# Kernel tuning notes

Hardware: AMD Instinct MI355X
Metric: run time of the kernel (lower is better)

Reference implementation:

```python
import jax, jax.numpy as jnp
import numpy as np

H = 1024
S = 2048
B = 16

def setup_inputs() -> dict:
    key = jax.random.key(0)
    k1, k2, k3, k4, k5, k6 = jax.random.split(key, 6)
    hidden = jax.random.normal(k1, (1, B, H), dtype=jnp.float32)
    encoder_outputs = jax.random.normal(k2, (S, B, H), dtype=jnp.float32)
    seq_mask = jax.random.randint(k3, (B, S), 0, 2, dtype=jnp.int32)
    # nn.Linear(2H, H): weight [H, 2H], bias [H]
    lim1 = 1.0 / np.sqrt(2 * H)
    attn_w = jax.random.uniform(k4, (H, 2 * H), minval=-lim1, maxval=lim1, dtype=jnp.float32)
    attn_b = jax.random.uniform(k5, (H,), minval=-lim1, maxval=lim1, dtype=jnp.float32)
    # nn.Linear(H, 1, bias=False): weight [1, H]
    lim2 = 1.0 / np.sqrt(H)
    score_w = jax.random.uniform(k6, (1, H), minval=-lim2, maxval=lim2, dtype=jnp.float32)
    return {"hidden": hidden, "encoder_outputs": encoder_outputs, "seq_mask": seq_mask,
            "attn_w": attn_w, "attn_b": attn_b, "score_w": score_w}

def reference(hidden, encoder_outputs, seq_mask, attn_w, attn_b, score_w):
    # Faithful to: cat([hidden.repeat(S,1,1), encoder_outputs], -1) @ attn_w.T + attn_b
    # Split the concat-linear into two GEMMs (identical math, avoids the big concat).
    h = hidden.shape[-1]
    Wh = attn_w[:, :h]   # acts on repeated hidden
    We = attn_w[:, h:]   # acts on encoder outputs
    # hidden: [1,B,H] broadcasts over S; encoder_outputs: [S,B,H]
    pre = jnp.einsum('obh,kh->obk', hidden, Wh) + jnp.einsum('sbh,kh->sbk', encoder_outputs, We) + attn_b
    proj = jnp.tanh(pre)                               # [S,B,H]
    energies = jnp.einsum('sbh,oh->sbo', proj, score_w)[..., 0]  # [S,B]
    energies = energies.T                              # [B,S] (transpose(0,1) in original)
    energies = jnp.where(seq_mask.astype(bool), jnp.float32(-1e12), energies)
    attn = jax.nn.softmax(energies, axis=1)            # [B,S]
    return attn[:, None, :]                            # [B,1,S]
```

## Files before the change

kernel.cpp:

```cpp
#include <hip/hip_runtime.h>
#include <hip/hip_bf16.h>

#define HDIM 1024
#define SEQ 2048
#define BATCH 16
#define M_TOT (SEQ*BATCH)
#define NBLK 4
#define BM 256
#define BN 256
#define BKT 64
#define NT (HDIM/BKT)

#define NB_ENC ((M_TOT*HDIM)/(8*256))
#define NB_WE  ((HDIM*HDIM)/(8*256))
#define NB_QK  (HDIM)

typedef __attribute__((ext_vector_type(8))) short short8;
typedef __attribute__((ext_vector_type(4))) float f32x4;

typedef const void __attribute__((address_space(1))) gvoid_t;
typedef void __attribute__((address_space(3))) svoid_t;
#define GLD16(gp, lp) __builtin_amdgcn_global_load_lds((gvoid_t*)(gp), (svoid_t*)(lp), 16, 0, 0)
#define VMC(N) asm volatile("s_waitcnt vmcnt(" #N ")" ::: "memory")

static __device__ __forceinline__ unsigned short f2bf(float f) {
    unsigned int x = __float_as_uint(f);
    unsigned int r = (x + 0x7FFFu + ((x >> 16) & 1u)) >> 16;
    return (unsigned short)r;
}

__global__ __launch_bounds__(256) void prep_all(const float* __restrict__ hidden,
                                                const float* __restrict__ enc,
                                                const float* __restrict__ attn_w,
                                                const float* __restrict__ attn_b,
                                                float* __restrict__ q,
                                                __hip_bfloat16* __restrict__ web,
                                                __hip_bfloat16* __restrict__ encb) {
    int bid = blockIdx.x;
    if (bid < NB_ENC) {
        size_t i0 = ((size_t)bid * 256 + threadIdx.x) * 8;
        const float4* s = reinterpret_cast<const float4*>(enc + i0);
        float4 a = s[0], b = s[1];
        union { unsigned short u[8]; short8 v; } cv;
        cv.u[0] = f2bf(a.x); cv.u[1] = f2bf(a.y); cv.u[2] = f2bf(a.z); cv.u[3] = f2bf(a.w);
        cv.u[4] = f2bf(b.x); cv.u[5] = f2bf(b.y); cv.u[6] = f2bf(b.z); cv.u[7] = f2bf(b.w);
        *reinterpret_cast<short8*>((unsigned short*)encb + i0) = cv.v;
        return;
    }
    if (bid < NB_ENC + NB_WE) {
        size_t i0 = ((size_t)(bid - NB_ENC) * 256 + threadIdx.x) * 8;
        int n = (int)(i0 >> 10);
        int h = (int)(i0 & 1023);
        const float4* src = reinterpret_cast<const float4*>(attn_w + (size_t)n * (2 * HDIM) + HDIM + h);
        float4 a = src[0], b = src[1];
        union { unsigned short u[8]; short8 v; } cv;
        cv.u[0] = f2bf(a.x); cv.u[1] = f2bf(a.y); cv.u[2] = f2bf(a.z); cv.u[3] = f2bf(a.w);
        cv.u[4] = f2bf(b.x); cv.u[5] = f2bf(b.y); cv.u[6] = f2bf(b.z); cv.u[7] = f2bf(b.w);
        *reinterpret_cast<short8*>((unsigned short*)web + i0) = cv.v;
        return;
    }
    int k = bid - (NB_ENC + NB_WE);
    int tid = threadIdx.x;
    const float* w = attn_w + (size_t)k * (2 * HDIM);
    float p[BATCH];
#pragma unroll
    for (int b = 0; b < BATCH; b++) p[b] = 0.f;
    for (int h = tid; h < HDIM; h += 256) {
        float wv = w[h];
#pragma unroll
        for (int b = 0; b < BATCH; b++) p[b] += hidden[b * HDIM + h] * wv;
    }
#pragma unroll
    for (int b = 0; b < BATCH; b++) {
        for (int off = 32; off; off >>= 1) p[b] += __shfl_down(p[b], off);
    }
    __shared__ float red[4][BATCH];
    int lane = tid & 63, wid = tid >> 6;
    if (lane == 0) {
#pragma unroll
        for (int b = 0; b < BATCH; b++) red[wid][b] = p[b];
    }
    __syncthreads();
    if (tid < BATCH) {
        float s = red[0][tid] + red[1][tid] + red[2][tid] + red[3][tid] + attn_b[k];
        q[(size_t)tid * HDIM + k] = s;
    }
}

__global__ __launch_bounds__(512, 2) void gemm8(const __hip_bfloat16* __restrict__ encb,
                                                const __hip_bfloat16* __restrict__ web,
                                                const float* __restrict__ qv,
                                                const float* __restrict__ score_w,
                                                float* __restrict__ part) {
    __shared__ __align__(16) char pool[131072];

    int tid = threadIdx.x;
    int lane = tid & 63;
    int wid = tid >> 6;
    int wr = wid >> 2;
    int wc = wid & 3;

    int bid = blockIdx.x;
    int lin = (bid & 7) * 64 + (bid >> 3);
    int bm = lin >> 2;
    int bn = lin & 3;
    int m0 = bm * BM, n0 = bn * BN;

    int srow = tid >> 3;
    int scolb = (((tid & 7) ^ ((tid >> 3) & 7)) << 4);
    const char* eb = (const char*)encb;
    const char* wb = (const char*)web;

    auto STG = [&](const char* g, int ldsoff) {
        GLD16(g + (size_t)srow * 2048 + scolb, pool + ldsoff + wid * 1024);
        GLD16(g + (size_t)(srow + 64) * 2048 + scolb, pool + ldsoff + 8192 + wid * 1024);
    };
    auto APTR = [&](int kt, int h) { return eb + ((size_t)(m0 + h * 128) * HDIM + kt * BKT) * 2; };
    auto BPTR = [&](int kt, int h) { return wb + ((size_t)(n0 + h * 128) * HDIM + kt * BKT) * 2; };
#define ALDS(par, h) ((par) * 32768 + (h) * 16384)
#define BLDS(par, h) (65536 + (par) * 32768 + (h) * 16384)

    int lq = lane & 15, lh = lane >> 4;
    int flip = (lane & 7) << 4;
    int pks0 = lq * 128 + ((lh * 16) ^ flip);
    int pks1 = lq * 128 + (((64 + lh * 16)) ^ flip);
    int aFB = wr * 16384;
    int bFB = 65536 + (wc >> 1) * 16384 + (wc & 1) * 8192;

    f32x4 acc[8][4];
#pragma unroll
    for (int i = 0; i < 8; i++)
#pragma unroll
        for (int j = 0; j < 4; j++) acc[i][j] = (f32x4)0.f;
    short8 br[4][2];

#define RD8(off) (*reinterpret_cast<const short8*>(pool + (off)))

#define PHASE(Q, PAR, STAGE_STMT, PRE_CLOSE)                                              \
    {                                                                                     \
        if ((Q) == 0) {                                                                   \
            _Pragma("unroll") for (int nj = 0; nj < 4; ++nj) {                            \
                br[nj][0] = RD8(bFB + (PAR) * 32768 + nj * 2048 + pks0);                  \
                br[nj][1] = RD8(bFB + (PAR) * 32768 + nj * 2048 + pks1);                  \
            }                                                                             \
        }                                                                                 \
        short8 a0k0 = RD8(aFB + (PAR) * 32768 + (2 * (Q)) * 2048 + pks0);                 \
        short8 a0k1 = RD8(aFB + (PAR) * 32768 + (2 * (Q)) * 2048 + pks1);                 \
        short8 a1k0 = RD8(aFB + (PAR) * 32768 + (2 * (Q) + 1) * 2048 + pks0);             \
        short8 a1k1 = RD8(aFB + (PAR) * 32768 + (2 * (Q) + 1) * 2048 + pks1);             \
        STAGE_STMT;                                                                       \
        __builtin_amdgcn_s_barrier();                                                     \
        __builtin_amdgcn_s_setprio(1);                                                    \
        _Pragma("unroll") for (int nj = 0; nj < 4; ++nj) {                                \
            acc[2 * (Q)][nj] = __builtin_amdgcn_mfma_f32_16x16x32_bf16(a0k0, br[nj][0], acc[2 * (Q)][nj], 0, 0, 0); \
            acc[2 * (Q)][nj] = __builtin_amdgcn_mfma_f32_16x16x32_bf16(a0k1, br[nj][1], acc[2 * (Q)][nj], 0, 0, 0); \
            acc[2 * (Q) + 1][nj] = __builtin_amdgcn_mfma_f32_16x16x32_bf16(a1k0, br[nj][0], acc[2 * (Q) + 1][nj], 0, 0, 0); \
            acc[2 * (Q) + 1][nj] = __builtin_amdgcn_mfma_f32_16x16x32_bf16(a1k1, br[nj][1], acc[2 * (Q) + 1][nj], 0, 0, 0); \
        }                                                                                 \
        __builtin_amdgcn_s_setprio(0);                                                    \
        PRE_CLOSE;                                                                        \
        __builtin_amdgcn_s_barrier();                                                     \
        __builtin_amdgcn_sched_barrier(0);                                                \
    }

    STG(BPTR(0, 0), BLDS(0, 0));
    STG(BPTR(0, 1), BLDS(0, 1));
    STG(APTR(0, 0), ALDS(0, 0));
    STG(APTR(0, 1), ALDS(0, 1));
    STG(BPTR(1, 0), BLDS(1, 0));
    STG(BPTR(1, 1), BLDS(1, 1));
    VMC(4);
    __builtin_amdgcn_s_barrier();
    __builtin_amdgcn_sched_barrier(0);

#pragma unroll 1
    for (int J = 0; J < 7; ++J) {
        int k1 = 2 * J + 1;
        PHASE(0, 0, STG(APTR(k1, 0), ALDS(1, 0)), );
        PHASE(1, 0, STG(APTR(k1, 1), ALDS(1, 1)), );
        PHASE(2, 0, STG(BPTR(k1 + 1, 0), BLDS(0, 0)), );
        PHASE(3, 0, STG(BPTR(k1 + 1, 1), BLDS(0, 1)), VMC(4));
        PHASE(0, 1, STG(APTR(k1 + 1, 0), ALDS(0, 0)), );
        PHASE(1, 1, STG(APTR(k1 + 1, 1), ALDS(0, 1)), );
        PHASE(2, 1, STG(BPTR(k1 + 2, 0), BLDS(1, 0)), );
        PHASE(3, 1, STG(BPTR(k1 + 2, 1), BLDS(1, 1)), VMC(4));
    }
    PHASE(0, 0, STG(APTR(15, 0), ALDS(1, 0)), );
    PHASE(1, 0, STG(APTR(15, 1), ALDS(1, 1)), );
    PHASE(2, 0, , );
    PHASE(3, 0, , VMC(0));
    PHASE(0, 1, , );
    PHASE(1, 1, , );
    PHASE(2, 1, , );
    PHASE(3, 1, , );

    float* q_lds = reinterpret_cast<float*>(pool);
    float* sc_lds = reinterpret_cast<float*>(pool + 16384);
    float* eng = reinterpret_cast<float*>(pool + 17408);
    {
        int qb = tid >> 5;
        int kl = (tid & 31) * 8;
        const float4* src = reinterpret_cast<const float4*>(qv + (size_t)qb * HDIM + n0 + kl);
        float4 v0 = src[0], v1 = src[1];
        *reinterpret_cast<float4*>(&q_lds[qb * 256 + kl]) = v0;
        *reinterpret_cast<float4*>(&q_lds[qb * 256 + kl + 4]) = v1;
        if (tid < BN) sc_lds[tid] = score_w[n0 + tid];
    }
    __syncthreads();

#pragma unroll
    for (int mi = 0; mi < 8; ++mi) {
#pragma unroll
        for (int r = 0; r < 4; ++r) {
            int b = lh * 4 + r;
            float s = 0.f;
#pragma unroll
            for (int nj = 0; nj < 4; ++nj) {
                int kl = wc * 64 + nj * 16 + lq;
                float v = acc[mi][nj][r] + q_lds[b * 256 + kl];
                float t = 1.f - 2.f / (__expf(2.f * v) + 1.f);
                s += sc_lds[kl] * t;
            }
            for (int off = 1; off < 16; off <<= 1) s += __shfl_xor(s, off);
            if (lq == 0) eng[wc * 256 + wr * 128 + mi * 16 + b] = s;
        }
    }
    __syncthreads();
    if (tid < BM) {
        float s = eng[tid] + eng[256 + tid] + eng[512 + tid] + eng[768 + tid];
        part[(size_t)bn * M_TOT + m0 + tid] = s;
    }
#undef PHASE
#undef RD8
#undef ALDS
#undef BLDS
}

__global__ __launch_bounds__(256) void softmax_kernel(const float* __restrict__ part,
                                                      const int* __restrict__ mask,
                                                      float* __restrict__ out) {
    int b = blockIdx.x;
    int tid = threadIdx.x;
    __shared__ float e_lds[SEQ];
    __shared__ float red[4], red2[4];
    int lane = tid & 63, wid = tid >> 6;
    float lmax = -3.4e38f;
    for (int it = 0; it < SEQ / 256; ++it) {
        int s = it * 256 + tid;
        size_t m = (size_t)s * BATCH + b;
        float e = 0.f;
#pragma unroll
        for (int c = 0; c < NBLK; c++) e += part[(size_t)c * M_TOT + m];
        if (mask[(size_t)b * SEQ + s]) e = -1e12f;
        e_lds[s] = e;
        lmax = fmaxf(lmax, e);
    }
    for (int off = 32; off; off >>= 1) lmax = fmaxf(lmax, __shfl_xor(lmax, off));
    if (lane == 0) red[wid] = lmax;
    __syncthreads();
    float gmax = fmaxf(fmaxf(red[0], red[1]), fmaxf(red[2], red[3]));
    float lsum = 0.f;
    for (int it = 0; it < SEQ / 256; ++it) {
        int s = it * 256 + tid;
        float p = __expf(e_lds[s] - gmax);
        e_lds[s] = p;
        lsum += p;
    }
    for (int off = 32; off; off >>= 1) lsum += __shfl_xor(lsum, off);
    if (lane == 0) red2[wid] = lsum;
    __syncthreads();
    float inv = 1.f / (red2[0] + red2[1] + red2[2] + red2[3]);
    for (int it = 0; it < SEQ / 256; ++it) {
        int s = it * 256 + tid;
        out[(size_t)b * SEQ + s] = e_lds[s] * inv;
    }
}

extern "C" void kernel_launch(void* const* d_in, const int* in_sizes, int n_in,
                              void* d_out, int out_size, void* d_ws, size_t ws_size,
                              hipStream_t stream) {
    const float* hidden   = (const float*)d_in[0];
    const float* enc      = (const float*)d_in[1];
    const int*   seq_mask = (const int*)d_in[2];
    const float* attn_w   = (const float*)d_in[3];
    const float* attn_b   = (const float*)d_in[4];
    const float* score_w  = (const float*)d_in[5];
    float* out = (float*)d_out;

    char* ws = (char*)d_ws;
    float* q = (float*)ws;
    __hip_bfloat16* web = (__hip_bfloat16*)(ws + 65536);
    float* part = (float*)(ws + 65536 + 2 * 1024 * 1024);
    __hip_bfloat16* encb = (__hip_bfloat16*)(ws + 65536 + 3 * 1024 * 1024);

    prep_all<<<dim3(NB_ENC + NB_WE + NB_QK), dim3(256), 0, stream>>>(hidden, enc, attn_w, attn_b, q, web, encb);
    gemm8<<<dim3(NBLK * (M_TOT / BM)), dim3(512), 0, stream>>>(encb, web, q, score_w, part);
    softmax_kernel<<<dim3(BATCH), dim3(256), 0, stream>>>(part, seq_mask, out);
}
```

Before: 120.7 us.

## Fuse fp32-to-bf16 encoder conversion into GEMM via fp32 LDS staging

Removes the separate pass that converts the 128 MB fp32 encoder tensor to bf16. The GEMM now streams fp32 encoder tiles directly into LDS and converts them to bf16 in registers before the MFMAs. To fit this it halves the K tile to 32, uses a triple-buffered pipeline and enlarges LDS to 144 KB. This drops one full read and a write-back of the encoder, at the price of twice the A-tile load bytes per GEMM and extra conversion ALU work. Because four N-blocks each re-read the fp32 A rows, global traffic grows, and the larger LDS footprint may limit occupancy.

```diff
diff --git a/kernel.cpp b/kernel.cpp
--- a/kernel.cpp
+++ b/kernel.cpp
@@ -8,10 +8,9 @@
 #define NBLK 4
 #define BM 256
 #define BN 256
-#define BKT 64
-#define NT (HDIM/BKT)
-
-#define NB_ENC ((M_TOT*HDIM)/(8*256))
+#define BKT 32
+#define NTT (HDIM/BKT)
+
 #define NB_WE  ((HDIM*HDIM)/(8*256))
 #define NB_QK  (HDIM)
 
@@ -30,25 +29,13 @@
 }
 
 __global__ __launch_bounds__(256) void prep_all(const float* __restrict__ hidden,
-                                                const float* __restrict__ enc,
                                                 const float* __restrict__ attn_w,
                                                 const float* __restrict__ attn_b,
                                                 float* __restrict__ q,
-                                                __hip_bfloat16* __restrict__ web,
-                                                __hip_bfloat16* __restrict__ encb) {
+                                                __hip_bfloat16* __restrict__ web) {
     int bid = blockIdx.x;
-    if (bid < NB_ENC) {
+    if (bid < NB_WE) {
         size_t i0 = ((size_t)bid * 256 + threadIdx.x) * 8;
-        const float4* s = reinterpret_cast<const float4*>(enc + i0);
-        float4 a = s[0], b = s[1];
-        union { unsigned short u[8]; short8 v; } cv;
-        cv.u[0] = f2bf(a.x); cv.u[1] = f2bf(a.y); cv.u[2] = f2bf(a.z); cv.u[3] = f2bf(a.w);
-        cv.u[4] = f2bf(b.x); cv.u[5] = f2bf(b.y); cv.u[6] = f2bf(b.z); cv.u[7] = f2bf(b.w);
-        *reinterpret_cast<short8*>((unsigned short*)encb + i0) = cv.v;
-        return;
-    }
-    if (bid < NB_ENC + NB_WE) {
-        size_t i0 = ((size_t)(bid - NB_ENC) * 256 + threadIdx.x) * 8;
         int n = (int)(i0 >> 10);
         int h = (int)(i0 & 1023);
         const float4* src = reinterpret_cast<const float4*>(attn_w + (size_t)n * (2 * HDIM) + HDIM + h);
@@ -59,7 +46,7 @@
         *reinterpret_cast<short8*>((unsigned short*)web + i0) = cv.v;
         return;
     }
-    int k = bid - (NB_ENC + NB_WE);
+    int k = bid - NB_WE;
     int tid = threadIdx.x;
     const float* w = attn_w + (size_t)k * (2 * HDIM);
     float p[BATCH];
@@ -87,12 +74,12 @@
     }
 }
 
-__global__ __launch_bounds__(512, 2) void gemm8(const __hip_bfloat16* __restrict__ encb,
+__global__ __launch_bounds__(512, 2) void gemm8(const float* __restrict__ enc,
                                                 const __hip_bfloat16* __restrict__ web,
                                                 const float* __restrict__ qv,
                                                 const float* __restrict__ score_w,
                                                 float* __restrict__ part) {
-    __shared__ __align__(16) char pool[131072];
+    __shared__ __align__(16) char pool[147456];
 
     int tid = threadIdx.x;
     int lane = tid & 63;
@@ -106,93 +93,108 @@
     int bn = lin & 3;
     int m0 = bm * BM, n0 = bn * BN;
 
-    int srow = tid >> 3;
-    int scolb = (((tid & 7) ^ ((tid >> 3) & 7)) << 4);
-    const char* eb = (const char*)encb;
-    const char* wb = (const char*)web;
-
-    auto STG = [&](const char* g, int ldsoff) {
-        GLD16(g + (size_t)srow * 2048 + scolb, pool + ldsoff + wid * 1024);
-        GLD16(g + (size_t)(srow + 64) * 2048 + scolb, pool + ldsoff + 8192 + wid * 1024);
+    const char* encB = (const char*)enc;
+    const char* webB = (const char*)web;
+
+    int arow_l = wid * 16 + (lane >> 3);
+    int agsw = ((lane & 7) ^ (lane >> 3)) << 4;
+    auto ASTG = [&](int t, int h, int ab) {
+        const char* g0 = encB + (((size_t)(m0 + h * 128 + arow_l) * HDIM + t * BKT) << 2) + agsw;
+        GLD16(g0, pool + ab * 32768 + h * 16384 + wid * 2048);
+        GLD16(g0 + (8u * HDIM << 2), pool + ab * 32768 + h * 16384 + wid * 2048 + 1024);
     };
-    auto APTR = [&](int kt, int h) { return eb + ((size_t)(m0 + h * 128) * HDIM + kt * BKT) * 2; };
-    auto BPTR = [&](int kt, int h) { return wb + ((size_t)(n0 + h * 128) * HDIM + kt * BKT) * 2; };
-#define ALDS(par, h) ((par) * 32768 + (h) * 16384)
-#define BLDS(par, h) (65536 + (par) * 32768 + (h) * 16384)
-
-    int lq = lane & 15, lh = lane >> 4;
-    int flip = (lane & 7) << 4;
-    int pks0 = lq * 128 + ((lh * 16) ^ flip);
-    int pks1 = lq * 128 + (((64 + lh * 16)) ^ flip);
-    int aFB = wr * 16384;
-    int bFB = 65536 + (wc >> 1) * 16384 + (wc & 1) * 8192;
+
+    int brow_l = wid * 16 + (lane >> 2);
+    int bgsw = ((lane & 3) ^ ((lane >> 2) & 3)) << 4;
+    auto BSTG = [&](int t, int h, int bb) {
+        const char* g0 = webB + (((size_t)(n0 + h * 128 + brow_l) * HDIM + t * BKT) << 1) + bgsw;
+        GLD16(g0, pool + 98304 + bb * 16384 + h * 8192 + wid * 1024);
+    };
+
+    int lq = lane & 15, kb = lane >> 4;
+    int aRB = wr * 16384 + lq * 128;
+    int aS0 = ((2 * kb) ^ (lq & 7)) << 4;
+    int aS1 = ((2 * kb + 1) ^ (lq & 7)) << 4;
+    int bRB = 98304 + (wc >> 1) * 8192 + ((wc & 1) * 64 + lq) * 64;
+    int bS = (kb ^ (lq & 3)) << 4;
 
     f32x4 acc[8][4];
 #pragma unroll
     for (int i = 0; i < 8; i++)
 #pragma unroll
         for (int j = 0; j < 4; j++) acc[i][j] = (f32x4)0.f;
-    short8 br[4][2];
+    short8 br[4];
 
 #define RD8(off) (*reinterpret_cast<const short8*>(pool + (off)))
-
-#define PHASE(Q, PAR, STAGE_STMT, PRE_CLOSE)                                              \
+#define RDF(off) (*reinterpret_cast<const f32x4*>(pool + (off)))
+
+    auto CVT = [&](f32x4 lo, f32x4 hi) {
+        union { __hip_bfloat162 b[4]; short8 s; } u;
+        u.b[0] = __float22bfloat162_rn(make_float2(lo[0], lo[1]));
+        u.b[1] = __float22bfloat162_rn(make_float2(lo[2], lo[3]));
+        u.b[2] = __float22bfloat162_rn(make_float2(hi[0], hi[1]));
+        u.b[3] = __float22bfloat162_rn(make_float2(hi[2], hi[3]));
+        return u.s;
+    };
+
+#define PH1(T, AB, SB, DOSTG)                                                             \
     {                                                                                     \
-        if ((Q) == 0) {                                                                   \
-            _Pragma("unroll") for (int nj = 0; nj < 4; ++nj) {                            \
-                br[nj][0] = RD8(bFB + (PAR) * 32768 + nj * 2048 + pks0);                  \
-                br[nj][1] = RD8(bFB + (PAR) * 32768 + nj * 2048 + pks1);                  \
-            }                                                                             \
-        }                                                                                 \
-        short8 a0k0 = RD8(aFB + (PAR) * 32768 + (2 * (Q)) * 2048 + pks0);                 \
-        short8 a0k1 = RD8(aFB + (PAR) * 32768 + (2 * (Q)) * 2048 + pks1);                 \
-        short8 a1k0 = RD8(aFB + (PAR) * 32768 + (2 * (Q) + 1) * 2048 + pks0);             \
-        short8 a1k1 = RD8(aFB + (PAR) * 32768 + (2 * (Q) + 1) * 2048 + pks1);             \
-        STAGE_STMT;                                                                       \
+        _Pragma("unroll") for (int nj = 0; nj < 4; ++nj)                                  \
+            br[nj] = RD8(bRB + (AB) * 16384 + nj * 1024 + bS);                            \
+        short8 af0 = CVT(RDF((AB) * 32768 + aRB + 0 * 2048 + aS0), RDF((AB) * 32768 + aRB + 0 * 2048 + aS1)); \
+        short8 af1 = CVT(RDF((AB) * 32768 + aRB + 1 * 2048 + aS0), RDF((AB) * 32768 + aRB + 1 * 2048 + aS1)); \
+        short8 af2 = CVT(RDF((AB) * 32768 + aRB + 2 * 2048 + aS0), RDF((AB) * 32768 + aRB + 2 * 2048 + aS1)); \
+        short8 af3 = CVT(RDF((AB) * 32768 + aRB + 3 * 2048 + aS0), RDF((AB) * 32768 + aRB + 3 * 2048 + aS1)); \
+        if (DOSTG) { ASTG((T) + 2, 0, SB); BSTG((T) + 2, 0, SB); }                        \
         __builtin_amdgcn_s_barrier();                                                     \
         __builtin_amdgcn_s_setprio(1);                                                    \
         _Pragma("unroll") for (int nj = 0; nj < 4; ++nj) {                                \
-            acc[2 * (Q)][nj] = __builtin_amdgcn_mfma_f32_16x16x32_bf16(a0k0, br[nj][0], acc[2 * (Q)][nj], 0, 0, 0); \
-            acc[2 * (Q)][nj] = __builtin_amdgcn_mfma_f32_16x16x32_bf16(a0k1, br[nj][1], acc[2 * (Q)][nj], 0, 0, 0); \
-            acc[2 * (Q) + 1][nj] = __builtin_amdgcn_mfma_f32_16x16x32_bf16(a1k0, br[nj][0], acc[2 * (Q) + 1][nj], 0, 0, 0); \
-            acc[2 * (Q) + 1][nj] = __builtin_amdgcn_mfma_f32_16x16x32_bf16(a1k1, br[nj][1], acc[2 * (Q) + 1][nj], 0, 0, 0); \
+            acc[0][nj] = __builtin_amdgcn_mfma_f32_16x16x32_bf16(af0, br[nj], acc[0][nj], 0, 0, 0); \
+            acc[1][nj] = __builtin_amdgcn_mfma_f32_16x16x32_bf16(af1, br[nj], acc[1][nj], 0, 0, 0); \
+            acc[2][nj] = __builtin_amdgcn_mfma_f32_16x16x32_bf16(af2, br[nj], acc[2][nj], 0, 0, 0); \
+            acc[3][nj] = __builtin_amdgcn_mfma_f32_16x16x32_bf16(af3, br[nj], acc[3][nj], 0, 0, 0); \
         }                                                                                 \
         __builtin_amdgcn_s_setprio(0);                                                    \
-        PRE_CLOSE;                                                                        \
         __builtin_amdgcn_s_barrier();                                                     \
         __builtin_amdgcn_sched_barrier(0);                                                \
     }
 
-    STG(BPTR(0, 0), BLDS(0, 0));
-    STG(BPTR(0, 1), BLDS(0, 1));
-    STG(APTR(0, 0), ALDS(0, 0));
-    STG(APTR(0, 1), ALDS(0, 1));
-    STG(BPTR(1, 0), BLDS(1, 0));
-    STG(BPTR(1, 1), BLDS(1, 1));
-    VMC(4);
+#define PH2(T, AB, SB, DOSTG, CLOSE)                                                      \
+    {                                                                                     \
+        short8 af4 = CVT(RDF((AB) * 32768 + aRB + 4 * 2048 + aS0), RDF((AB) * 32768 + aRB + 4 * 2048 + aS1)); \
+        short8 af5 = CVT(RDF((AB) * 32768 + aRB + 5 * 2048 + aS0), RDF((AB) * 32768 + aRB + 5 * 2048 + aS1)); \
+        short8 af6 = CVT(RDF((AB) * 32768 + aRB + 6 * 2048 + aS0), RDF((AB) * 32768 + aRB + 6 * 2048 + aS1)); \
+        short8 af7 = CVT(RDF((AB) * 32768 + aRB + 7 * 2048 + aS0), RDF((AB) * 32768 + aRB + 7 * 2048 + aS1)); \
+        if (DOSTG) { ASTG((T) + 2, 1, SB); BSTG((T) + 2, 1, SB); }                        \
+        __builtin_amdgcn_s_barrier();                                                     \
+        __builtin_amdgcn_s_setprio(1);                                                    \
+        _Pragma("unroll") for (int nj = 0; nj < 4; ++nj) {                                \
+            acc[4][nj] = __builtin_amdgcn_mfma_f32_16x16x32_bf16(af4, br[nj], acc[4][nj], 0, 0, 0); \
+            acc[5][nj] = __builtin_amdgcn_mfma_f32_16x16x32_bf16(af5, br[nj], acc[5][nj], 0, 0, 0); \
+            acc[6][nj] = __builtin_amdgcn_mfma_f32_16x16x32_bf16(af6, br[nj], acc[6][nj], 0, 0, 0); \
+            acc[7][nj] = __builtin_amdgcn_mfma_f32_16x16x32_bf16(af7, br[nj], acc[7][nj], 0, 0, 0); \
+        }                                                                                 \
+        __builtin_amdgcn_s_setprio(0);                                                    \
+        CLOSE;                                                                            \
+        __builtin_amdgcn_s_barrier();                                                     \
+        __builtin_amdgcn_sched_barrier(0);                                                \
+    }
+
+    ASTG(0, 0, 0); ASTG(0, 1, 0); BSTG(0, 0, 0); BSTG(0, 1, 0);
+    ASTG(1, 0, 1); ASTG(1, 1, 1); BSTG(1, 0, 1); BSTG(1, 1, 1);
+    VMC(6);
     __builtin_amdgcn_s_barrier();
     __builtin_amdgcn_sched_barrier(0);
 
 #pragma unroll 1
-    for (int J = 0; J < 7; ++J) {
-        int k1 = 2 * J + 1;
-        PHASE(0, 0, STG(APTR(k1, 0), ALDS(1, 0)), );
-        PHASE(1, 0, STG(APTR(k1, 1), ALDS(1, 1)), );
-        PHASE(2, 0, STG(BPTR(k1 + 1, 0), BLDS(0, 0)), );
-        PHASE(3, 0, STG(BPTR(k1 + 1, 1), BLDS(0, 1)), VMC(4));
-        PHASE(0, 1, STG(APTR(k1 + 1, 0), ALDS(0, 0)), );
-        PHASE(1, 1, STG(APTR(k1 + 1, 1), ALDS(0, 1)), );
-        PHASE(2, 1, STG(BPTR(k1 + 2, 0), BLDS(1, 0)), );
-        PHASE(3, 1, STG(BPTR(k1 + 2, 1), BLDS(1, 1)), VMC(4));
-    }
-    PHASE(0, 0, STG(APTR(15, 0), ALDS(1, 0)), );
-    PHASE(1, 0, STG(APTR(15, 1), ALDS(1, 1)), );
-    PHASE(2, 0, , );
-    PHASE(3, 0, , VMC(0));
-    PHASE(0, 1, , );
-    PHASE(1, 1, , );
-    PHASE(2, 1, , );
-    PHASE(3, 1, , );
+    for (int J = 0; J < 10; ++J) {
+        int t0 = 3 * J;
+        PH1(t0, 0, 2, 1);     PH2(t0, 0, 2, 1, VMC(6));
+        PH1(t0 + 1, 1, 0, 1); PH2(t0 + 1, 1, 0, 1, VMC(6));
+        PH1(t0 + 2, 2, 1, 1); PH2(t0 + 2, 2, 1, 1, VMC(6));
+    }
+    PH1(30, 0, 0, 0); PH2(30, 0, 0, 0, VMC(0));
+    PH1(31, 1, 0, 0); PH2(31, 1, 0, 0, );
 
     float* q_lds = reinterpret_cast<float*>(pool);
     float* sc_lds = reinterpret_cast<float*>(pool + 16384);
@@ -208,6 +210,7 @@
     }
     __syncthreads();
 
+    int lh = lane >> 4;
 #pragma unroll
     for (int mi = 0; mi < 8; ++mi) {
 #pragma unroll
@@ -230,10 +233,10 @@
         float s = eng[tid] + eng[256 + tid] + eng[512 + tid] + eng[768 + tid];
         part[(size_t)bn * M_TOT + m0 + tid] = s;
     }
-#undef PHASE
+#undef PH1
+#undef PH2
 #undef RD8
-#undef ALDS
-#undef BLDS
+#undef RDF
 }
 
 __global__ __launch_bounds__(256) void softmax_kernel(const float* __restrict__ part,
@@ -291,9 +294,8 @@
     float* q = (float*)ws;
     __hip_bfloat16* web = (__hip_bfloat16*)(ws + 65536);
     float* part = (float*)(ws + 65536 + 2 * 1024 * 1024);
-    __hip_bfloat16* encb = (__hip_bfloat16*)(ws + 65536 + 3 * 1024 * 1024);
-
-    prep_all<<<dim3(NB_ENC + NB_WE + NB_QK), dim3(256), 0, stream>>>(hidden, enc, attn_w, attn_b, q, web, encb);
-    gemm8<<<dim3(NBLK * (M_TOT / BM)), dim3(512), 0, stream>>>(encb, web, q, score_w, part);
+
+    prep_all<<<dim3(NB_WE + NB_QK), dim3(256), 0, stream>>>(hidden, attn_w, attn_b, q, web);
+    gemm8<<<dim3(NBLK * (M_TOT / BM)), dim3(512), 0, stream>>>(enc, web, q, score_w, part);
     softmax_kernel<<<dim3(BATCH), dim3(256), 0, stream>>>(part, seq_mask, out);
 }
```

New measurement: 124.3 us. 3.0% more time.

## Triple-buffer B tiles in LDS and drop per-cluster barriers in GEMM loop

Applied to the files above, without the earlier changes.

Grows the LDS pool from 128KB to 160KB so the weight (B) tile gets three buffers while the encoder (A) tile stays double-buffered. The main loop is restructured into tiles that each run four MFMA clusters with no barrier between clusters, leaving one barrier per K-tile instead of two per phase. B loads are now issued two K-steps ahead, which keeps reads and writes on different buffers without intra-tile syncs. The aim is to cut barrier stalls and give loads more latency slack. The cost is extra LDS pressure, which could limit occupancy if more than one block per CU had been resident.

```diff
diff --git a/kernel.cpp b/kernel.cpp
--- a/kernel.cpp
+++ b/kernel.cpp
@@ -92,7 +92,7 @@
                                                 const float* __restrict__ qv,
                                                 const float* __restrict__ score_w,
                                                 float* __restrict__ part) {
-    __shared__ __align__(16) char pool[131072];
+    __shared__ __align__(16) char pool[163840];
 
     int tid = threadIdx.x;
     int lane = tid & 63;
@@ -118,14 +118,14 @@
     auto APTR = [&](int kt, int h) { return eb + ((size_t)(m0 + h * 128) * HDIM + kt * BKT) * 2; };
     auto BPTR = [&](int kt, int h) { return wb + ((size_t)(n0 + h * 128) * HDIM + kt * BKT) * 2; };
 #define ALDS(par, h) ((par) * 32768 + (h) * 16384)
-#define BLDS(par, h) (65536 + (par) * 32768 + (h) * 16384)
+#define BLDS(buf, h) (65536 + (buf) * 32768 + (h) * 16384)
 
     int lq = lane & 15, lh = lane >> 4;
     int flip = (lane & 7) << 4;
     int pks0 = lq * 128 + ((lh * 16) ^ flip);
     int pks1 = lq * 128 + (((64 + lh * 16)) ^ flip);
     int aFB = wr * 16384;
-    int bFB = 65536 + (wc >> 1) * 16384 + (wc & 1) * 8192;
+    int bOFF = (wc >> 1) * 16384 + (wc & 1) * 8192;
 
     f32x4 acc[8][4];
 #pragma unroll
@@ -136,12 +136,12 @@
 
 #define RD8(off) (*reinterpret_cast<const short8*>(pool + (off)))
 
-#define PHASE(Q, PAR, STAGE_STMT, PRE_CLOSE)                                              \
+#define CLUSTER(Q, PAR, BB, STAGE_STMT)                                                   \
     {                                                                                     \
         if ((Q) == 0) {                                                                   \
             _Pragma("unroll") for (int nj = 0; nj < 4; ++nj) {                            \
-                br[nj][0] = RD8(bFB + (PAR) * 32768 + nj * 2048 + pks0);                  \
-                br[nj][1] = RD8(bFB + (PAR) * 32768 + nj * 2048 + pks1);                  \
+                br[nj][0] = RD8(65536 + (BB) * 32768 + bOFF + nj * 2048 + pks0);          \
+                br[nj][1] = RD8(65536 + (BB) * 32768 + bOFF + nj * 2048 + pks1);          \
             }                                                                             \
         }                                                                                 \
         short8 a0k0 = RD8(aFB + (PAR) * 32768 + (2 * (Q)) * 2048 + pks0);                 \
@@ -149,7 +149,6 @@
         short8 a1k0 = RD8(aFB + (PAR) * 32768 + (2 * (Q) + 1) * 2048 + pks0);             \
         short8 a1k1 = RD8(aFB + (PAR) * 32768 + (2 * (Q) + 1) * 2048 + pks1);             \
         STAGE_STMT;                                                                       \
-        __builtin_amdgcn_s_barrier();                                                     \
         __builtin_amdgcn_s_setprio(1);                                                    \
         _Pragma("unroll") for (int nj = 0; nj < 4; ++nj) {                                \
             acc[2 * (Q)][nj] = __builtin_amdgcn_mfma_f32_16x16x32_bf16(a0k0, br[nj][0], acc[2 * (Q)][nj], 0, 0, 0); \
@@ -158,15 +157,23 @@
             acc[2 * (Q) + 1][nj] = __builtin_amdgcn_mfma_f32_16x16x32_bf16(a1k1, br[nj][1], acc[2 * (Q) + 1][nj], 0, 0, 0); \
         }                                                                                 \
         __builtin_amdgcn_s_setprio(0);                                                    \
-        PRE_CLOSE;                                                                        \
+    }
+
+#define TILE(PAR, BB, S1, S2, S3, S4, CLOSE)                                              \
+    {                                                                                     \
+        CLUSTER(0, PAR, BB, S1);                                                          \
+        CLUSTER(1, PAR, BB, S2);                                                          \
+        CLUSTER(2, PAR, BB, S3);                                                          \
+        CLUSTER(3, PAR, BB, S4);                                                          \
+        CLOSE;                                                                            \
         __builtin_amdgcn_s_barrier();                                                     \
         __builtin_amdgcn_sched_barrier(0);                                                \
     }
 
+    STG(APTR(0, 0), ALDS(0, 0));
+    STG(APTR(0, 1), ALDS(0, 1));
     STG(BPTR(0, 0), BLDS(0, 0));
     STG(BPTR(0, 1), BLDS(0, 1));
-    STG(APTR(0, 0), ALDS(0, 0));
-    STG(APTR(0, 1), ALDS(0, 1));
     STG(BPTR(1, 0), BLDS(1, 0));
     STG(BPTR(1, 1), BLDS(1, 1));
     VMC(4);
@@ -174,25 +181,27 @@
     __builtin_amdgcn_sched_barrier(0);
 
 #pragma unroll 1
-    for (int J = 0; J < 7; ++J) {
-        int k1 = 2 * J + 1;
-        PHASE(0, 0, STG(APTR(k1, 0), ALDS(1, 0)), );
-        PHASE(1, 0, STG(APTR(k1, 1), ALDS(1, 1)), );
-        PHASE(2, 0, STG(BPTR(k1 + 1, 0), BLDS(0, 0)), );
-        PHASE(3, 0, STG(BPTR(k1 + 1, 1), BLDS(0, 1)), VMC(4));
-        PHASE(0, 1, STG(APTR(k1 + 1, 0), ALDS(0, 0)), );
-        PHASE(1, 1, STG(APTR(k1 + 1, 1), ALDS(0, 1)), );
-        PHASE(2, 1, STG(BPTR(k1 + 2, 0), BLDS(1, 0)), );
-        PHASE(3, 1, STG(BPTR(k1 + 2, 1), BLDS(1, 1)), VMC(4));
-    }
-    PHASE(0, 0, STG(APTR(15, 0), ALDS(1, 0)), );
-    PHASE(1, 0, STG(APTR(15, 1), ALDS(1, 1)), );
-    PHASE(2, 0, , );
-    PHASE(3, 0, , VMC(0));
-    PHASE(0, 1, , );
-    PHASE(1, 1, , );
-    PHASE(2, 1, , );
-    PHASE(3, 1, , );
+    for (int J = 0; J < 2; ++J) {
+        int t = 6 * J;
+        TILE(0, 0, STG(APTR(t + 1, 0), ALDS(1, 0)), STG(APTR(t + 1, 1), ALDS(1, 1)),
+                   STG(BPTR(t + 2, 0), BLDS(2, 0)), STG(BPTR(t + 2, 1), BLDS(2, 1)), VMC(4));
+        TILE(1, 1, STG(APTR(t + 2, 0), ALDS(0, 0)), STG(APTR(t + 2, 1), ALDS(0, 1)),
+                   STG(BPTR(t + 3, 0), BLDS(0, 0)), STG(BPTR(t + 3, 1), BLDS(0, 1)), VMC(4));
+        TILE(0, 2, STG(APTR(t + 3, 0), ALDS(1, 0)), STG(APTR(t + 3, 1), ALDS(1, 1)),
+                   STG(BPTR(t + 4, 0), BLDS(1, 0)), STG(BPTR(t + 4, 1), BLDS(1, 1)), VMC(4));
+        TILE(1, 0, STG(APTR(t + 4, 0), ALDS(0, 0)), STG(APTR(t + 4, 1), ALDS(0, 1)),
+                   STG(BPTR(t + 5, 0), BLDS(2, 0)), STG(BPTR(t + 5, 1), BLDS(2, 1)), VMC(4));
+        TILE(0, 1, STG(APTR(t + 5, 0), ALDS(1, 0)), STG(APTR(t + 5, 1), ALDS(1, 1)),
+                   STG(BPTR(t + 6, 0), BLDS(0, 0)), STG(BPTR(t + 6, 1), BLDS(0, 1)), VMC(4));
+        TILE(1, 2, STG(APTR(t + 6, 0), ALDS(0, 0)), STG(APTR(t + 6, 1), ALDS(0, 1)),
+                   STG(BPTR(t + 7, 0), BLDS(1, 0)), STG(BPTR(t + 7, 1), BLDS(1, 1)), VMC(4));
+    }
+    TILE(0, 0, STG(APTR(13, 0), ALDS(1, 0)), STG(APTR(13, 1), ALDS(1, 1)),
+               STG(BPTR(14, 0), BLDS(2, 0)), STG(BPTR(14, 1), BLDS(2, 1)), VMC(4));
+    TILE(1, 1, STG(APTR(14, 0), ALDS(0, 0)), STG(APTR(14, 1), ALDS(0, 1)),
+               STG(BPTR(15, 0), BLDS(0, 0)), STG(BPTR(15, 1), BLDS(0, 1)), VMC(4));
+    TILE(0, 2, STG(APTR(15, 0), ALDS(1, 0)), STG(APTR(15, 1), ALDS(1, 1)), , , VMC(0));
+    TILE(1, 0, , , , , );
 
     float* q_lds = reinterpret_cast<float*>(pool);
     float* sc_lds = reinterpret_cast<float*>(pool + 16384);
@@ -230,7 +239,8 @@
         float s = eng[tid] + eng[256 + tid] + eng[512 + tid] + eng[768 + tid];
         part[(size_t)bn * M_TOT + m0 + tid] = s;
     }
-#undef PHASE
+#undef CLUSTER
+#undef TILE
 #undef RD8
 #undef ALDS
 #undef BLDS
```

After: 118.6 us (median of 2 runs). About the same (-1.7%).
